# Optimization experiments

Hardware: AMD Instinct MI355X
Metric: run time of the kernel (lower is better)

## Reference

```python
import math
import jax, jax.numpy as jnp
import numpy as np

NQ, NK = 16384, 4096
QDIM, KDIM, MID = 512, 256, 256


def setup_inputs() -> dict:
    key = jax.random.key(0)
    k1, k2, k3, k4, k5, k6, k7, k8 = jax.random.split(key, 8)
    return {
        "global_embeddings": jax.random.normal(k1, (NQ, QDIM), dtype=jnp.float32),
        "substruct_embeddings": jax.random.normal(k2, (NK, KDIM), dtype=jnp.float32),
        "substruct_weight": jax.random.uniform(k3, (NK,), dtype=jnp.float32),
        "mask": jax.random.randint(k4, (NQ, NK), 0, 2, dtype=jnp.int32),
        "Wq": jax.random.normal(k5, (MID, QDIM), dtype=jnp.float32) / math.sqrt(QDIM),
        "bq": jax.random.normal(k6, (MID,), dtype=jnp.float32) * 0.01,
        "Wk": jax.random.normal(k7, (MID, KDIM), dtype=jnp.float32) / math.sqrt(KDIM),
        "bk": jax.random.normal(k8, (MID,), dtype=jnp.float32) * 0.01,
    }


def reference(global_embeddings, substruct_embeddings, substruct_weight, mask, Wq, bq, Wk, bk):
    # Q/K projections (torch Linear: x @ W.T + b)
    Q = global_embeddings @ Wq.T + bq            # [NQ, MID]
    K = substruct_embeddings @ Wk.T + bk         # [NK, MID]
    scores = (Q @ K.T) / math.sqrt(MID)          # [NQ, NK]
    scores = jnp.where(mask == 0, -jnp.inf, scores)
    attn = jax.nn.softmax(scores, axis=-1)       # row-wise stable softmax
    # torch.diag(w) @ E  ==  elementwise row scaling
    V = substruct_weight[:, None] * substruct_embeddings  # [NK, KDIM]
    return attn @ V                              # [NQ, KDIM]
```

## Files before the change

kernel.cpp:

```cpp
#include <hip/hip_runtime.h>
#include <hip/hip_bf16.h>

typedef __bf16 bf16_t;
typedef bf16_t bf16x8 __attribute__((ext_vector_type(8)));
typedef float  f32x4  __attribute__((ext_vector_type(4)));
typedef unsigned long long u64;

#define MFMA16(A,B,C) __builtin_amdgcn_mfma_f32_16x16x32_bf16((A),(B),(C),0,0,0)


template<int KA>
__global__ __launch_bounds__(256)
void proj_kernel(const float* __restrict__ A, const float* __restrict__ W,
                 const float* __restrict__ b, bf16_t* __restrict__ C,
                 float scale)
{
    __shared__ bf16_t Alds[64][40];
    __shared__ bf16_t Wlds[256][40];

    const int t  = threadIdx.x;
    const int w  = t >> 6, l = t & 63, lr = l & 15, lg = l >> 4;
    const int m0 = blockIdx.x * 64;

    f32x4 acc[16];
#pragma unroll
    for (int tt = 0; tt < 16; ++tt) acc[tt] = (f32x4){0.f, 0.f, 0.f, 0.f};

    const int ar  = t >> 2;
    const int ac8 = (t & 3) * 8;

    for (int kb = 0; kb < KA / 32; ++kb) {
        {
            const float* ap = A + (size_t)(m0 + ar) * KA + kb * 32 + ac8;
            float4 a0 = *(const float4*)ap;
            float4 a1 = *(const float4*)(ap + 4);
            bf16x8 av;
            av[0]=(bf16_t)a0.x; av[1]=(bf16_t)a0.y; av[2]=(bf16_t)a0.z; av[3]=(bf16_t)a0.w;
            av[4]=(bf16_t)a1.x; av[5]=(bf16_t)a1.y; av[6]=(bf16_t)a1.z; av[7]=(bf16_t)a1.w;
            *(bf16x8*)&Alds[ar][ac8] = av;
        }
#pragma unroll
        for (int c = 0; c < 4; ++c) {
            int e8 = c * 256 + t;
            int wr = e8 >> 2, wc8 = (e8 & 3) * 8;
            const float* wp = W + (size_t)wr * KA + kb * 32 + wc8;
            float4 w0 = *(const float4*)wp;
            float4 w1 = *(const float4*)(wp + 4);
            bf16x8 wv;
            wv[0]=(bf16_t)w0.x; wv[1]=(bf16_t)w0.y; wv[2]=(bf16_t)w0.z; wv[3]=(bf16_t)w0.w;
            wv[4]=(bf16_t)w1.x; wv[5]=(bf16_t)w1.y; wv[6]=(bf16_t)w1.z; wv[7]=(bf16_t)w1.w;
            *(bf16x8*)&Wlds[wr][wc8] = wv;
        }
        __syncthreads();

        bf16x8 af = *(bf16x8*)&Alds[w * 16 + lr][lg * 8];
#pragma unroll
        for (int tt = 0; tt < 16; ++tt) {
            bf16x8 bfrag = *(bf16x8*)&Wlds[tt * 16 + lr][lg * 8];
            acc[tt] = MFMA16(af, bfrag, acc[tt]);
        }
        __syncthreads();
    }

#pragma unroll
    for (int tt = 0; tt < 16; ++tt) {
        int col = tt * 16 + lr;
        float bias = b[col];
#pragma unroll
        for (int r = 0; r < 4; ++r) {
            int row = m0 + w * 16 + lg * 4 + r;
            C[(size_t)row * 256 + col] = (bf16_t)((acc[tt][r] + bias) * scale);
        }
    }
}

__global__ __launch_bounds__(256)
void buildvt_kernel(const float* __restrict__ S, const float* __restrict__ wgt,
                    bf16_t* __restrict__ VT)
{
    int i = blockIdx.x * 256 + threadIdx.x;
    int d = i >> 12, k = i & 4095;
    VT[i] = (bf16_t)(wgt[k] * S[(size_t)k * 256 + d]);
}

template<bool SPLIT>
__global__ __launch_bounds__(256, 2)
void attn_kernel(const bf16_t* __restrict__ Qb, const bf16_t* __restrict__ Kb,
                 const bf16_t* __restrict__ VT, const int* __restrict__ mask,
                 float* __restrict__ out, float* __restrict__ pacc,
                 float* __restrict__ pm, float* __restrict__ pl)
{
    __shared__ bf16_t Klds[64][264];
    __shared__ bf16_t VTlds[256][72];
    __shared__ bf16_t Plds[64][72];

    const int t  = threadIdx.x;
    const int w  = t >> 6, l = t & 63, lr = l & 15, lg = l >> 4;
    const int q0 = blockIdx.x * 64;
    const int qw = q0 + w * 16;
    const int half = SPLIT ? (int)blockIdx.y : 0;
    const int NT   = SPLIT ? 32 : 64;
    const int kb0  = half * NT;

    bf16x8 qf[8];
    {
        const bf16_t* qrow = Qb + (size_t)(qw + lr) * 256;
#pragma unroll
        for (int kk = 0; kk < 8; ++kk)
            qf[kk] = *(const bf16x8*)(qrow + kk * 32 + lg * 8);
    }

    bf16x8 vone;
#pragma unroll
    for (int j = 0; j < 8; ++j) vone[j] = (bf16_t)1.0f;

    f32x4 acc[16];
#pragma unroll
    for (int dt = 0; dt < 16; ++dt) acc[dt] = (f32x4){0.f, 0.f, 0.f, 0.f};
    f32x4 lacc = (f32x4){0.f, 0.f, 0.f, 0.f};
    float mrow[4];
#pragma unroll
    for (int r = 0; r < 4; ++r) mrow[r] = -1e30f;

    for (int tb = 0; tb < NT; ++tb) {
        const int kb = kb0 + tb;

        int4 mv[4];
#pragma unroll
        for (int r = 0; r < 4; ++r)
            mv[r] = *(const int4*)(mask + (size_t)(qw + 4 * lg + r) * 4096
                                   + kb * 64 + lr * 4);

#pragma unroll
        for (int c = 0; c < 8; ++c) {
            int e8 = c * 256 + t;
            int krow = e8 >> 5, kc8 = (e8 & 31) * 8;
            *(bf16x8*)&Klds[krow][kc8] =
                *(const bf16x8*)(Kb + (size_t)(kb * 64 + krow) * 256 + kc8);
        }
#pragma unroll
        for (int c = 0; c < 8; ++c) {
            int e8 = c * 256 + t;
            int d = e8 >> 3, c8 = (e8 & 7) * 8;
            *(bf16x8*)&VTlds[d][c8] =
                *(const bf16x8*)(VT + (size_t)d * 4096 + kb * 64 + c8);
        }

        u64 rowbits[4];
#pragma unroll
        for (int r = 0; r < 4; ++r) {
            u64 b0 = __ballot(mv[r].x != 0);
            u64 b1 = __ballot(mv[r].y != 0);
            u64 b2 = __ballot(mv[r].z != 0);
            u64 b3 = __ballot(mv[r].w != 0);
            u64 w01  = (lr & 1) ? b1 : b0;
            u64 w23  = (lr & 1) ? b3 : b2;
            u64 wsel = (lr & 2) ? w23 : w01;
            rowbits[r] = wsel >> (lg * 16 + (lr >> 2));
        }
        __syncthreads();

        f32x4 s[4];
#pragma unroll
        for (int tt = 0; tt < 4; ++tt) {
            f32x4 sv = (f32x4){0.f, 0.f, 0.f, 0.f};
#pragma unroll
            for (int kk = 0; kk < 8; ++kk) {
                bf16x8 kf = *(bf16x8*)&Klds[tt * 16 + lr][kk * 32 + lg * 8];
                sv = MFMA16(qf[kk], kf, sv);
            }
            s[tt] = sv;
        }
#pragma unroll
        for (int tt = 0; tt < 4; ++tt)
#pragma unroll
            for (int r = 0; r < 4; ++r) {
                bool keep = ((rowbits[r] >> (4 * tt)) & 1ull) != 0;
                s[tt][r] = keep ? s[tt][r] : -1e30f;
            }

        float bm[4];
#pragma unroll
        for (int r = 0; r < 4; ++r)
            bm[r] = fmaxf(fmaxf(s[0][r], s[1][r]), fmaxf(s[2][r], s[3][r]));
#pragma unroll
        for (int off = 1; off < 16; off <<= 1)
#pragma unroll
            for (int r = 0; r < 4; ++r)
                bm[r] = fmaxf(bm[r], __shfl_xor(bm[r], off));

        bool need = false;
#pragma unroll
        for (int r = 0; r < 4; ++r) need = need || (bm[r] > mrow[r] + 8.f);
        if (__any(need)) {
#pragma unroll
            for (int r = 0; r < 4; ++r) {
                float mn = fmaxf(mrow[r], bm[r]);
                float fr = __expf(mrow[r] - mn);
                mrow[r] = mn;
                lacc[r] *= fr;
#pragma unroll
                for (int dt = 0; dt < 16; ++dt) acc[dt][r] *= fr;
            }
        }

#pragma unroll
        for (int tt = 0; tt < 4; ++tt)
#pragma unroll
            for (int r = 0; r < 4; ++r)
                Plds[w * 16 + lg * 4 + r][tt * 16 + lr]
                    = (bf16_t)__expf(s[tt][r] - mrow[r]);
        asm volatile("s_waitcnt lgkmcnt(0)" ::: "memory");
        __builtin_amdgcn_sched_barrier(0);

        bf16x8 pa0 = *(bf16x8*)&Plds[w * 16 + lr][lg * 8];
        bf16x8 pa1 = *(bf16x8*)&Plds[w * 16 + lr][32 + lg * 8];
        lacc = MFMA16(pa0, vone, lacc);
        lacc = MFMA16(pa1, vone, lacc);
#pragma unroll
        for (int dt = 0; dt < 16; ++dt) {
            bf16x8 v0 = *(bf16x8*)&VTlds[dt * 16 + lr][lg * 8];
            bf16x8 v1 = *(bf16x8*)&VTlds[dt * 16 + lr][32 + lg * 8];
            acc[dt] = MFMA16(pa0, v0, acc[dt]);
            acc[dt] = MFMA16(pa1, v1, acc[dt]);
        }
        __syncthreads();
    }

    if (SPLIT) {
        float* pa = pacc + (size_t)half * 16384 * 256;
#pragma unroll
        for (int r = 0; r < 4; ++r) {
            int row = qw + lg * 4 + r;
#pragma unroll
            for (int dt = 0; dt < 16; ++dt)
                pa[(size_t)row * 256 + dt * 16 + lr] = acc[dt][r];
            if (lr == 0) {
                pm[half * 16384 + row] = mrow[r];
                pl[half * 16384 + row] = lacc[r];
            }
        }
    } else {
#pragma unroll
        for (int r = 0; r < 4; ++r) {
            float inv = 1.0f / lacc[r];
#pragma unroll
            for (int dt = 0; dt < 16; ++dt)
                out[(size_t)(qw + lg * 4 + r) * 256 + dt * 16 + lr] = acc[dt][r] * inv;
        }
    }
}

__global__ __launch_bounds__(256)
void combine_kernel(const float* __restrict__ pacc, const float* __restrict__ pm,
                    const float* __restrict__ pl, float* __restrict__ out)
{
    int idx = blockIdx.x * 256 + threadIdx.x;
    int row = idx >> 6, c4 = (idx & 63) * 4;
    float m0 = pm[row], m1 = pm[16384 + row];
    float l0 = pl[row], l1 = pl[16384 + row];
    float m  = fmaxf(m0, m1);
    float a  = __expf(m0 - m), b = __expf(m1 - m);
    float inv = 1.0f / (l0 * a + l1 * b);
    float4 x0 = *(const float4*)(pacc + (size_t)row * 256 + c4);
    float4 x1 = *(const float4*)(pacc + (size_t)16384 * 256 + (size_t)row * 256 + c4);
    float4 o;
    o.x = (x0.x * a + x1.x * b) * inv;
    o.y = (x0.y * a + x1.y * b) * inv;
    o.z = (x0.z * a + x1.z * b) * inv;
    o.w = (x0.w * a + x1.w * b) * inv;
    *(float4*)(out + (size_t)row * 256 + c4) = o;
}

extern "C" void kernel_launch(void* const* d_in, const int* in_sizes, int n_in,
                              void* d_out, int out_size, void* d_ws, size_t ws_size,
                              hipStream_t stream)
{
    const float* gE   = (const float*)d_in[0];
    const float* sE   = (const float*)d_in[1];
    const float* wgt  = (const float*)d_in[2];
    const int*   mask = (const int*)  d_in[3];
    const float* Wq   = (const float*)d_in[4];
    const float* bq   = (const float*)d_in[5];
    const float* Wk   = (const float*)d_in[6];
    const float* bk   = (const float*)d_in[7];
    float* out = (float*)d_out;

    char* ws = (char*)d_ws;
    bf16_t* Qb = (bf16_t*)ws;
    bf16_t* Kb = (bf16_t*)(ws + 8388608);
    bf16_t* VT = (bf16_t*)(ws + 10485760);
    float*  pacc = (float*)(ws + 12582912);
    float*  pm   = (float*)(ws + 46137344);
    float*  pl   = (float*)(ws + 46268416);
    const size_t need_full = 46399488;
    const size_t need_min  = 12582912;

    if (ws_size < need_min) return;

    proj_kernel<512><<<dim3(256, 1), 256, 0, stream>>>(gE, Wq, bq, Qb, 0.0625f);
    proj_kernel<256><<<dim3(64, 1), 256, 0, stream>>>(sE, Wk, bk, Kb, 1.0f);
    buildvt_kernel<<<4096, 256, 0, stream>>>(sE, wgt, VT);

    if (ws_size >= need_full) {
        attn_kernel<true><<<dim3(256, 2), 256, 0, stream>>>(
            Qb, Kb, VT, mask, out, pacc, pm, pl);
        combine_kernel<<<4096, 256, 0, stream>>>(pacc, pm, pl, out);
    } else {
        attn_kernel<false><<<dim3(256, 1), 256, 0, stream>>>(
            Qb, Kb, VT, mask, out, nullptr, nullptr, nullptr);
    }
}
```

Before: 217.9 us.

## Load K/V tiles directly to LDS with pre-swizzled global layouts

K and V^T tiles are now copied with global_load_lds (direct global-to-LDS DMA) instead of going through registers. The padded LDS arrays are replaced by unpadded ones that use an XOR swizzle to avoid bank conflicts. Because the direct loads cannot permute data, the swizzle is baked into the global layout by the K projection and buildvt kernels. The P tile also gets an XOR swizzle. This cuts VGPR use and load-issue instructions in the attention loop, at the cost of coupling the producer kernels' layouts to the consumer.

```diff
diff --git a/kernel.cpp b/kernel.cpp
--- a/kernel.cpp
+++ b/kernel.cpp
@@ -5,11 +5,18 @@
 typedef bf16_t bf16x8 __attribute__((ext_vector_type(8)));
 typedef float  f32x4  __attribute__((ext_vector_type(4)));
 typedef unsigned long long u64;
+typedef unsigned int u32;
 
 #define MFMA16(A,B,C) __builtin_amdgcn_mfma_f32_16x16x32_bf16((A),(B),(C),0,0,0)
 
 
-template<int KA>
+static __device__ __forceinline__ void gl_lds16(const bf16_t* g, void* l) {
+    __builtin_amdgcn_global_load_lds(
+        (const __attribute__((address_space(1))) u32*)(const void*)g,
+        (__attribute__((address_space(3))) u32*)l, 16, 0, 0);
+}
+
+template<int KA, bool SWZ>
 __global__ __launch_bounds__(256)
 void proj_kernel(const float* __restrict__ A, const float* __restrict__ W,
                  const float* __restrict__ b, bf16_t* __restrict__ C,
@@ -69,7 +76,9 @@
 #pragma unroll
         for (int r = 0; r < 4; ++r) {
             int row = m0 + w * 16 + lg * 4 + r;
-            C[(size_t)row * 256 + col] = (bf16_t)((acc[tt][r] + bias) * scale);
+            int colS = col;
+            if (SWZ) colS = (((col >> 3) ^ (row & 7)) << 3) | (col & 7);
+            C[(size_t)row * 256 + colS] = (bf16_t)((acc[tt][r] + bias) * scale);
         }
     }
 }
@@ -80,7 +89,8 @@
 {
     int i = blockIdx.x * 256 + threadIdx.x;
     int d = i >> 12, k = i & 4095;
-    VT[i] = (bf16_t)(wgt[k] * S[(size_t)k * 256 + d]);
+    int kt = (k & ~63) | (((((k >> 3) & 7) ^ (d & 7)) << 3)) | (k & 7);
+    VT[i] = (bf16_t)(wgt[kt] * S[(size_t)kt * 256 + d]);
 }
 
 template<bool SPLIT>
@@ -90,9 +100,9 @@
                  float* __restrict__ out, float* __restrict__ pacc,
                  float* __restrict__ pm, float* __restrict__ pl)
 {
-    __shared__ bf16_t Klds[64][264];
-    __shared__ bf16_t VTlds[256][72];
-    __shared__ bf16_t Plds[64][72];
+    __shared__ __align__(16) char Kraw[32768];
+    __shared__ __align__(16) char Vraw[32768];
+    __shared__ __align__(16) char Praw[8192];
 
     const int t  = threadIdx.x;
     const int w  = t >> 6, l = t & 63, lr = l & 15, lg = l >> 4;
@@ -132,18 +142,16 @@
                                    + kb * 64 + lr * 4);
 
 #pragma unroll
-        for (int c = 0; c < 8; ++c) {
-            int e8 = c * 256 + t;
-            int krow = e8 >> 5, kc8 = (e8 & 31) * 8;
-            *(bf16x8*)&Klds[krow][kc8] =
-                *(const bf16x8*)(Kb + (size_t)(kb * 64 + krow) * 256 + kc8);
-        }
-#pragma unroll
-        for (int c = 0; c < 8; ++c) {
-            int e8 = c * 256 + t;
-            int d = e8 >> 3, c8 = (e8 & 7) * 8;
-            *(bf16x8*)&VTlds[d][c8] =
-                *(const bf16x8*)(VT + (size_t)d * 4096 + kb * 64 + c8);
+        for (int i = 0; i < 8; ++i) {
+            int row = w * 16 + i * 2 + (l >> 5);
+            gl_lds16(Kb + (size_t)(kb * 64 + row) * 256 + (l & 31) * 8,
+                     Kraw + (w * 16 + i * 2) * 512);
+        }
+#pragma unroll
+        for (int i = 0; i < 8; ++i) {
+            int d = w * 64 + i * 8 + (l >> 3);
+            gl_lds16(VT + (size_t)d * 4096 + kb * 64 + (l & 7) * 8,
+                     Vraw + (w * 64 + i * 8) * 128);
         }
 
         u64 rowbits[4];
@@ -166,7 +174,8 @@
             f32x4 sv = (f32x4){0.f, 0.f, 0.f, 0.f};
 #pragma unroll
             for (int kk = 0; kk < 8; ++kk) {
-                bf16x8 kf = *(bf16x8*)&Klds[tt * 16 + lr][kk * 32 + lg * 8];
+                bf16x8 kf = *(bf16x8*)(Kraw + (((tt * 16 + lr) * 512)
+                                | ((((kk * 4 + lg) ^ (lr & 7)) << 4))));
                 sv = MFMA16(qf[kk], kf, sv);
             }
             s[tt] = sv;
@@ -207,20 +216,32 @@
 #pragma unroll
         for (int tt = 0; tt < 4; ++tt)
 #pragma unroll
-            for (int r = 0; r < 4; ++r)
-                Plds[w * 16 + lg * 4 + r][tt * 16 + lr]
+            for (int r = 0; r < 4; ++r) {
+                int prow = w * 16 + lg * 4 + r;
+                *(bf16_t*)(Praw + ((prow * 128 + (tt * 16 + lr) * 2)
+                                   ^ ((prow & 7) << 4)))
                     = (bf16_t)__expf(s[tt][r] - mrow[r]);
+            }
         asm volatile("s_waitcnt lgkmcnt(0)" ::: "memory");
         __builtin_amdgcn_sched_barrier(0);
 
-        bf16x8 pa0 = *(bf16x8*)&Plds[w * 16 + lr][lg * 8];
-        bf16x8 pa1 = *(bf16x8*)&Plds[w * 16 + lr][32 + lg * 8];
+        bf16x8 pa0, pa1;
+        {
+            int prow = w * 16 + lr;
+            pa0 = *(bf16x8*)(Praw + ((prow * 128 + (0 * 4 + lg) * 16)
+                                     ^ ((prow & 7) << 4)));
+            pa1 = *(bf16x8*)(Praw + ((prow * 128 + (1 * 4 + lg) * 16)
+                                     ^ ((prow & 7) << 4)));
+        }
         lacc = MFMA16(pa0, vone, lacc);
         lacc = MFMA16(pa1, vone, lacc);
 #pragma unroll
         for (int dt = 0; dt < 16; ++dt) {
-            bf16x8 v0 = *(bf16x8*)&VTlds[dt * 16 + lr][lg * 8];
-            bf16x8 v1 = *(bf16x8*)&VTlds[dt * 16 + lr][32 + lg * 8];
+            int vrow = dt * 16 + lr;
+            bf16x8 v0 = *(bf16x8*)(Vraw + ((vrow * 128)
+                            | ((((0 * 4 + lg) ^ (lr & 7)) << 4))));
+            bf16x8 v1 = *(bf16x8*)(Vraw + ((vrow * 128)
+                            | ((((1 * 4 + lg) ^ (lr & 7)) << 4))));
             acc[dt] = MFMA16(pa0, v0, acc[dt]);
             acc[dt] = MFMA16(pa1, v1, acc[dt]);
         }
@@ -298,8 +319,8 @@
 
     if (ws_size < need_min) return;
 
-    proj_kernel<512><<<dim3(256, 1), 256, 0, stream>>>(gE, Wq, bq, Qb, 0.0625f);
-    proj_kernel<256><<<dim3(64, 1), 256, 0, stream>>>(sE, Wk, bk, Kb, 1.0f);
+    proj_kernel<512, false><<<dim3(256, 1), 256, 0, stream>>>(gE, Wq, bq, Qb, 0.0625f);
+    proj_kernel<256, true ><<<dim3(64, 1), 256, 0, stream>>>(sE, Wk, bk, Kb, 1.0f);
     buildvt_kernel<<<4096, 256, 0, stream>>>(sE, wgt, VT);
 
     if (ws_size >= need_full) {
```

Result: faster. 210.5 us (-3.4%).
